# Kernel optimization log

Measured on AMD Instinct MI355X. Metric: run time of the kernel, lower is better.

The kernel has to match this reference:

```python
import jax, jax.numpy as jnp
import numpy as np

K = 2  # top-k experts per token

def setup_inputs() -> dict:
    key = jax.random.key(0)
    ks = jax.random.split(key, 8)
    B, S, D, F, E = 2, 1024, 1024, 4096, 8
    s_in = 1.0 / np.sqrt(D)
    s_mid = 1.0 / np.sqrt(F)
    return {
        "x": jax.random.normal(ks[0], (B, S, D), dtype=jnp.float32),
        "Wr": jax.random.uniform(ks[1], (D, E), jnp.float32, -s_in, s_in),
        "br": jax.random.uniform(ks[2], (E,), jnp.float32, -s_in, s_in),
        "W1": jax.random.uniform(ks[3], (E, D, F), jnp.float32, -s_in, s_in),
        "b1": jax.random.uniform(ks[4], (E, F), jnp.float32, -s_in, s_in),
        "W2": jax.random.uniform(ks[5], (E, F, D), jnp.float32, -s_mid, s_mid),
        "b2": jax.random.uniform(ks[6], (E, D), jnp.float32, -s_mid, s_mid),
    }

def _moe(x, Wr, br, W1, b1, W2, b2):
    E = Wr.shape[1]
    # router (eval mode: no noise)
    logits = jnp.einsum('bsd,de->bse', x, Wr) + br          # [B,S,E]
    topk_logits, topk_idx = jax.lax.top_k(logits, K)        # [B,S,K]
    router_probs = jax.nn.softmax(topk_logits, axis=-1)     # [B,S,K]
    # per-expert combine weight: sum over k slots assigned to expert e
    onehot = jax.nn.one_hot(topk_idx, E, dtype=x.dtype)     # [B,S,K,E]
    w = jnp.einsum('bske,bsk->bse', onehot, router_probs)   # [B,S,E]
    # scan over experts (fixed small E), accumulate weighted expert outputs
    def step(acc, ew):
        W1j, b1j, W2j, b2j, wj = ew                          # wj: [B,S]
        h = jax.nn.gelu(jnp.einsum('bsd,df->bsf', x, W1j) + b1j, approximate=False)
        y = jnp.einsum('bsf,fd->bsd', h, W2j) + b2j
        return acc + y * wj[..., None], None
    out, _ = jax.lax.scan(step, jnp.zeros_like(x),
                          (W1, b1, W2, b2, jnp.transpose(w, (2, 0, 1))))
    return out, router_probs

def reference(x, Wr, br, W1, b1, W2, b2):
    return _moe(x, Wr, br, W1, b1, W2, b2)
```

## Files before the change

### kernel.cpp

```cpp
#include <hip/hip_runtime.h>
#include <hip/hip_bf16.h>
#include <cstdint>

#define TOKENS 2048
#define Dm 1024
#define Fm 4096
#define Em 8

typedef short s16x8 __attribute__((ext_vector_type(8)));
typedef float f32x4 __attribute__((ext_vector_type(4)));

#define GLOAD16(g, l) __builtin_amdgcn_global_load_lds(                     \
    (const __attribute__((address_space(1))) void*)(g),                     \
    (__attribute__((address_space(3))) void*)(l), 16, 0, 0)

__device__ __forceinline__ ushort f2bf(float f) {
  union { float f; uint32_t u; } v; v.f = f;
  uint32_t r = v.u + 0x7fffu + ((v.u >> 16) & 1u);
  return (ushort)(r >> 16);
}

__global__ void transcvt(const float* __restrict__ in, ushort* __restrict__ out,
                         int R, int C) {
  __shared__ float tile[32][33];
  int e = blockIdx.z;
  const float* src = in + (size_t)e * R * C;
  ushort* dst = out + (size_t)e * R * C;
  int c0 = blockIdx.x * 32, r0 = blockIdx.y * 32;
  int lr = threadIdx.x >> 5, lc = threadIdx.x & 31;
#pragma unroll
  for (int p = 0; p < 4; ++p) {
    int r = r0 + p * 8 + lr;
    tile[p * 8 + lr][lc] = src[(size_t)r * C + c0 + lc];
  }
  __syncthreads();
#pragma unroll
  for (int p = 0; p < 4; ++p) {
    int c = c0 + p * 8 + lr;
    dst[(size_t)c * R + r0 + lc] = f2bf(tile[lc][p * 8 + lr]);
  }
}

__global__ void router(const float* __restrict__ x, const float* __restrict__ Wr,
                       const float* __restrict__ br, float* __restrict__ probs,
                       int* __restrict__ e_sel, float* __restrict__ w_sel,
                       ushort* __restrict__ xb) {
  int t = blockIdx.x;
  const float4* xr4 = (const float4*)(x + (size_t)t * Dm);
  float4 v = xr4[threadIdx.x];
  ushort4 o;
  o.x = f2bf(v.x); o.y = f2bf(v.y); o.z = f2bf(v.z); o.w = f2bf(v.w);
  ((ushort4*)(xb + (size_t)t * Dm))[threadIdx.x] = o;

  int d0 = threadIdx.x * 4;
  const float4* wr4 = (const float4*)(Wr + (size_t)d0 * Em);
  float wv[4][8];
#pragma unroll
  for (int r = 0; r < 4; ++r) {
    float4 a = wr4[r * 2], b = wr4[r * 2 + 1];
    wv[r][0] = a.x; wv[r][1] = a.y; wv[r][2] = a.z; wv[r][3] = a.w;
    wv[r][4] = b.x; wv[r][5] = b.y; wv[r][6] = b.z; wv[r][7] = b.w;
  }
  float xs[4] = {v.x, v.y, v.z, v.w};
  float acc[Em];
#pragma unroll
  for (int e = 0; e < Em; ++e)
    acc[e] = xs[0] * wv[0][e] + xs[1] * wv[1][e] + xs[2] * wv[2][e] + xs[3] * wv[3][e];

#pragma unroll
  for (int off = 32; off >= 1; off >>= 1)
#pragma unroll
    for (int e = 0; e < Em; ++e) acc[e] += __shfl_down(acc[e], off);
  __shared__ float red[4][Em];
  int lane = threadIdx.x & 63, wid = threadIdx.x >> 6;
  if (lane == 0)
#pragma unroll
    for (int e = 0; e < Em; ++e) red[wid][e] = acc[e];
  __syncthreads();
  if (threadIdx.x == 0) {
    float lg[Em];
#pragma unroll
    for (int e = 0; e < Em; ++e)
      lg[e] = red[0][e] + red[1][e] + red[2][e] + red[3][e] + br[e];
    int i0 = 0;
    for (int e = 1; e < Em; ++e) if (lg[e] > lg[i0]) i0 = e;
    int i1 = -1;
    for (int e = 0; e < Em; ++e) {
      if (e == i0) continue;
      if (i1 < 0 || lg[e] > lg[i1]) i1 = e;
    }
    float d = lg[i1] - lg[i0];
    float tt = expf(d);
    float inv = 1.f / (1.f + tt);
    float p0 = inv, p1 = tt * inv;
    probs[t * 2] = p0; probs[t * 2 + 1] = p1;
    e_sel[t * 2] = i0; e_sel[t * 2 + 1] = i1;
    w_sel[t * 2] = p0; w_sel[t * 2 + 1] = p1;
  }
}

__global__ void build_lists(const int* __restrict__ e_sel, const float* __restrict__ w_sel,
                            int* __restrict__ tok_of_row, float* __restrict__ w_of_row,
                            int* __restrict__ base, int* __restrict__ npad,
                            int* __restrict__ ncnt) {
  __shared__ int cnt[Em], run[Em], sbase[Em];
  __shared__ int wsum[4][Em];
  int tid = threadIdx.x, lane = tid & 63, wid = tid >> 6;
  if (tid < Em) { cnt[tid] = 0; run[tid] = 0; }
  __syncthreads();
  for (int t = tid; t < TOKENS; t += 256) {
    atomicAdd(&cnt[e_sel[2 * t]], 1);
    atomicAdd(&cnt[e_sel[2 * t + 1]], 1);
  }
  __syncthreads();
  if (tid == 0) {
    int b = 0;
    for (int e = 0; e < Em; ++e) {
      base[e] = b; sbase[e] = b;
      int n = cnt[e]; ncnt[e] = n;
      int p = (n + 127) & ~127;
      npad[e] = p; b += p;
    }
  }
  __syncthreads();
  for (int c = 0; c < TOKENS / 256; ++c) {
    int t = c * 256 + tid;
    int e0 = e_sel[2 * t], e1 = e_sel[2 * t + 1];
    unsigned long long mm[Em];
#pragma unroll
    for (int e = 0; e < Em; ++e) {
      unsigned long long m0 = __ballot(e0 == e);
      unsigned long long m1 = __ballot(e1 == e);
      mm[e] = m0 | m1;
      if (lane == 0) wsum[wid][e] = __popcll(mm[e]);
    }
    __syncthreads();
    unsigned long long below = (1ull << lane) - 1ull;
    {
      int e = e0;
      int p = __popcll(mm[e] & below);
      int pre = 0;
      for (int w = 0; w < wid; ++w) pre += wsum[w][e];
      int row = sbase[e] + run[e] + pre + p;
      tok_of_row[row] = t; w_of_row[row] = w_sel[2 * t];
    }
    {
      int e = e1;
      int p = __popcll(mm[e] & below);
      int pre = 0;
      for (int w = 0; w < wid; ++w) pre += wsum[w][e];
      int row = sbase[e] + run[e] + pre + p;
      tok_of_row[row] = t; w_of_row[row] = w_sel[2 * t + 1];
    }
    __syncthreads();
    if (tid < Em) {
      int s = 0;
      for (int w = 0; w < 4; ++w) s += wsum[w][tid];
      run[tid] += s;
    }
    __syncthreads();
  }
  for (int e = 0; e < Em; ++e) {
    int n = cnt[e];
    int p = (n + 127) & ~127;
    for (int i = n + tid; i < p; i += 256) {
      tok_of_row[sbase[e] + i] = -1;
      w_of_row[sbase[e] + i] = 0.f;
    }
  }
}

__global__ void out_init(const int* __restrict__ e_sel, const float* __restrict__ w_sel,
                         const float* __restrict__ b2, float* __restrict__ out) {
  int t = blockIdx.x;
  int e0 = e_sel[2 * t], e1 = e_sel[2 * t + 1];
  float w0 = w_sel[2 * t], w1 = w_sel[2 * t + 1];
  const float4* p0 = (const float4*)(b2 + (size_t)e0 * Dm);
  const float4* p1 = (const float4*)(b2 + (size_t)e1 * Dm);
  float4* o = (float4*)(out + (size_t)t * Dm);
  for (int i = threadIdx.x; i < Dm / 4; i += 256) {
    float4 a = p0[i], b = p1[i];
    float4 r;
    r.x = w0 * a.x + w1 * b.x; r.y = w0 * a.y + w1 * b.y;
    r.z = w0 * a.z + w1 * b.z; r.w = w0 * a.w + w1 * b.w;
    o[i] = r;
  }
}

__global__ __launch_bounds__(256) void gemm1(
    const ushort* __restrict__ xb, const ushort* __restrict__ bmat,
    const float* __restrict__ b1, ushort* __restrict__ H,
    const int* __restrict__ tok_of_row, const int* __restrict__ base,
    const int* __restrict__ npad) {
  int e = blockIdx.y >> 4, rt = blockIdx.y & 15;
  int np = npad[e];
  if (rt * 128 >= np) return;
  int row0 = base[e] + rt * 128;
  int n0 = blockIdx.x * 128;
  __shared__ ushort As[128 * 32];
  __shared__ ushort Bs[128 * 32];
  __shared__ int toks[128];
  int tid = threadIdx.x, lane = tid & 63, wid = tid >> 6;
  if (tid < 128) toks[tid] = tok_of_row[row0 + tid];
  __syncthreads();
  int arow = tid >> 2, asub = tid & 3;
  int t0 = toks[arow];      if (t0 < 0) t0 = 0;
  int t1 = toks[64 + arow]; if (t1 < 0) t1 = 0;
  const ushort* sA0 = xb + (size_t)t0 * Dm + asub * 8;
  const ushort* sA1 = xb + (size_t)t1 * Dm + asub * 8;
  const ushort* sB0 = bmat + ((size_t)e * Fm + n0 + arow) * Dm + asub * 8;
  const ushort* sB1 = sB0 + (size_t)64 * Dm;
  char* ldA0 = (char*)As + wid * 1024;
  char* ldA1 = (char*)As + 4096 + wid * 1024;
  char* ldB0 = (char*)Bs + wid * 1024;
  char* ldB1 = (char*)Bs + 4096 + wid * 1024;
  int wr = wid >> 1, wc = wid & 1;
  const ushort* aB = As + ((size_t)(wr * 64 + (lane & 15)) * 32) + (lane >> 4) * 8;
  const ushort* bB = Bs + ((size_t)(wc * 64 + (lane & 15)) * 32) + (lane >> 4) * 8;
  f32x4 acc[4][4] = {};
  for (int kt = 0; kt < Dm / 32; ++kt) {
    GLOAD16(sA0, ldA0);
    GLOAD16(sA1, ldA1);
    GLOAD16(sB0, ldB0);
    GLOAD16(sB1, ldB1);
    sA0 += 32; sA1 += 32; sB0 += 32; sB1 += 32;
    __syncthreads();
    s16x8 av[4], bv[4];
#pragma unroll
    for (int m = 0; m < 4; ++m) av[m] = *(const s16x8*)(aB + m * 512);
#pragma unroll
    for (int n = 0; n < 4; ++n) bv[n] = *(const s16x8*)(bB + n * 512);
#pragma unroll
    for (int m = 0; m < 4; ++m)
#pragma unroll
      for (int n = 0; n < 4; ++n)
        acc[m][n] = __builtin_amdgcn_mfma_f32_16x16x32_bf16(av[m], bv[n], acc[m][n], 0, 0, 0);
    __syncthreads();
  }
  int rb = wr * 64 + ((lane >> 4) << 2);
  int cb = n0 + wc * 64 + (lane & 15);
#pragma unroll
  for (int n = 0; n < 4; ++n) {
    int col = cb + n * 16;
    float bias = b1[e * Fm + col];
#pragma unroll
    for (int m = 0; m < 4; ++m) {
      int r = row0 + rb + m * 16;
#pragma unroll
      for (int j = 0; j < 4; ++j) {
        float v = acc[m][n][j] + bias;
        float g = 0.5f * v * (1.f + erff(v * 0.70710678118654752f));
        H[(size_t)(r + j) * Fm + col] = f2bf(g);
      }
    }
  }
}

__global__ __launch_bounds__(256) void gemm2(
    const ushort* __restrict__ H, const ushort* __restrict__ bmat,
    const int* __restrict__ tok_of_row, const float* __restrict__ w_of_row,
    const int* __restrict__ base, const int* __restrict__ npad,
    float* __restrict__ out) {
  int e = blockIdx.y >> 4, rt = blockIdx.y & 15;
  int np = npad[e];
  if (rt * 128 >= np) return;
  int row0 = base[e] + rt * 128;
  int n0 = blockIdx.x * 128;
  int k0 = blockIdx.z * (Fm / 2);
  __shared__ ushort As[128 * 32];
  __shared__ ushort Bs[128 * 32];
  __shared__ int toks[128];
  __shared__ float wts[128];
  int tid = threadIdx.x, lane = tid & 63, wid = tid >> 6;
  if (tid < 128) {
    toks[tid] = tok_of_row[row0 + tid];
    wts[tid] = w_of_row[row0 + tid];
  }
  __syncthreads();
  int arow = tid >> 2, asub = tid & 3;
  const ushort* sA0 = H + (size_t)(row0 + arow) * Fm + k0 + asub * 8;
  const ushort* sA1 = sA0 + (size_t)64 * Fm;
  const ushort* sB0 = bmat + ((size_t)e * Dm + n0 + arow) * Fm + k0 + asub * 8;
  const ushort* sB1 = sB0 + (size_t)64 * Fm;
  char* ldA0 = (char*)As + wid * 1024;
  char* ldA1 = (char*)As + 4096 + wid * 1024;
  char* ldB0 = (char*)Bs + wid * 1024;
  char* ldB1 = (char*)Bs + 4096 + wid * 1024;
  int wr = wid >> 1, wc = wid & 1;
  const ushort* aB = As + ((size_t)(wr * 64 + (lane & 15)) * 32) + (lane >> 4) * 8;
  const ushort* bB = Bs + ((size_t)(wc * 64 + (lane & 15)) * 32) + (lane >> 4) * 8;
  f32x4 acc[4][4] = {};
  for (int kt = 0; kt < Fm / 2 / 32; ++kt) {
    GLOAD16(sA0, ldA0);
    GLOAD16(sA1, ldA1);
    GLOAD16(sB0, ldB0);
    GLOAD16(sB1, ldB1);
    sA0 += 32; sA1 += 32; sB0 += 32; sB1 += 32;
    __syncthreads();
    s16x8 av[4], bv[4];
#pragma unroll
    for (int m = 0; m < 4; ++m) av[m] = *(const s16x8*)(aB + m * 512);
#pragma unroll
    for (int n = 0; n < 4; ++n) bv[n] = *(const s16x8*)(bB + n * 512);
#pragma unroll
    for (int m = 0; m < 4; ++m)
#pragma unroll
      for (int n = 0; n < 4; ++n)
        acc[m][n] = __builtin_amdgcn_mfma_f32_16x16x32_bf16(av[m], bv[n], acc[m][n], 0, 0, 0);
    __syncthreads();
  }
  int rb = wr * 64 + ((lane >> 4) << 2);
  int cb = n0 + wc * 64 + (lane & 15);
#pragma unroll
  for (int n = 0; n < 4; ++n) {
    int col = cb + n * 16;
#pragma unroll
    for (int m = 0; m < 4; ++m) {
      int rl = rb + m * 16;
#pragma unroll
      for (int j = 0; j < 4; ++j) {
        int tok = toks[rl + j];
        if (tok >= 0)
          atomicAdd(&out[(size_t)tok * Dm + col], wts[rl + j] * acc[m][n][j]);
      }
    }
  }
}

extern "C" void kernel_launch(void* const* d_in, const int* in_sizes, int n_in,
                              void* d_out, int out_size, void* d_ws, size_t ws_size,
                              hipStream_t stream) {
  const float* x  = (const float*)d_in[0];
  const float* Wr = (const float*)d_in[1];
  const float* br = (const float*)d_in[2];
  const float* W1 = (const float*)d_in[3];
  const float* b1 = (const float*)d_in[4];
  const float* W2 = (const float*)d_in[5];
  const float* b2 = (const float*)d_in[6];
  float* out = (float*)d_out;
  float* probs = out + (size_t)TOKENS * Dm;

  char* ws = (char*)d_ws;
  ushort* Wt   = (ushort*)ws;
  ushort* Hbuf = (ushort*)(ws + 67108864);
  ushort* xb   = (ushort*)(ws + 109051904);
  int*   tok_of_row = (int*)(ws + 113246208);
  float* w_of_row   = (float*)(ws + 113266688);
  int*   e_sel      = (int*)(ws + 113287168);
  float* w_sel      = (float*)(ws + 113303552);
  int*   meta       = (int*)(ws + 113319936);

  transcvt<<<dim3(Fm / 32, Dm / 32, Em), 256, 0, stream>>>(W1, Wt, Dm, Fm);
  router<<<TOKENS, 256, 0, stream>>>(x, Wr, br, probs, e_sel, w_sel, xb);
  build_lists<<<1, 256, 0, stream>>>(e_sel, w_sel, tok_of_row, w_of_row,
                                     meta, meta + 8, meta + 16);
  out_init<<<TOKENS, 256, 0, stream>>>(e_sel, w_sel, b2, out);
  gemm1<<<dim3(32, 128), 256, 0, stream>>>(xb, Wt, b1, Hbuf, tok_of_row,
                                           meta, meta + 8);
  transcvt<<<dim3(Dm / 32, Fm / 32, Em), 256, 0, stream>>>(W2, Wt, Fm, Dm);
  gemm2<<<dim3(8, 128, 2), 256, 0, stream>>>(Hbuf, Wt, tok_of_row, w_of_row,
                                             meta, meta + 8, out);
}
```

Baseline: 275.7 us.

## Fuse prep kernels, overlap W2 transpose with gemm1 idle blocks, widen K-tile with swizzle

Merges the W1 transpose with the router into one launch, and merges list building with the output bias init into another. When the workspace is large enough, the W2 transpose/convert is done by gemm1's idle (unused expert-tile) blocks instead of a separate kernel. Both GEMMs now load a 64-wide K slice per stage into a 128x64 XOR-swizzled LDS tile to cut bank conflicts and halve barrier count. gemm1 stages its GELU output through LDS so H is written with 16-byte coalesced stores. The trade-offs are more LDS per block, which may lower occupancy, and load imbalance from idle blocks doing the transpose work.

```diff
diff --git a/kernel.cpp b/kernel.cpp
--- a/kernel.cpp
+++ b/kernel.cpp
@@ -22,30 +22,43 @@
 
 __global__ void transcvt(const float* __restrict__ in, ushort* __restrict__ out,
                          int R, int C) {
-  __shared__ float tile[32][33];
+  __shared__ float tile[32 * 33];
   int e = blockIdx.z;
   const float* src = in + (size_t)e * R * C;
   ushort* dst = out + (size_t)e * R * C;
   int c0 = blockIdx.x * 32, r0 = blockIdx.y * 32;
   int lr = threadIdx.x >> 5, lc = threadIdx.x & 31;
 #pragma unroll
-  for (int p = 0; p < 4; ++p) {
-    int r = r0 + p * 8 + lr;
-    tile[p * 8 + lr][lc] = src[(size_t)r * C + c0 + lc];
-  }
-  __syncthreads();
-#pragma unroll
-  for (int p = 0; p < 4; ++p) {
-    int c = c0 + p * 8 + lr;
-    dst[(size_t)c * R + r0 + lc] = f2bf(tile[lc][p * 8 + lr]);
-  }
-}
-
-__global__ void router(const float* __restrict__ x, const float* __restrict__ Wr,
-                       const float* __restrict__ br, float* __restrict__ probs,
-                       int* __restrict__ e_sel, float* __restrict__ w_sel,
-                       ushort* __restrict__ xb) {
-  int t = blockIdx.x;
+  for (int p = 0; p < 4; ++p)
+    tile[(p * 8 + lr) * 33 + lc] = src[(size_t)(r0 + p * 8 + lr) * C + c0 + lc];
+  __syncthreads();
+#pragma unroll
+  for (int p = 0; p < 4; ++p)
+    dst[(size_t)(c0 + p * 8 + lr) * R + r0 + lc] = f2bf(tile[lc * 33 + p * 8 + lr]);
+}
+
+__global__ void prep(const float* __restrict__ W1, ushort* __restrict__ W1T,
+                     const float* __restrict__ x, const float* __restrict__ Wr,
+                     const float* __restrict__ br, float* __restrict__ probs,
+                     int* __restrict__ e_sel, float* __restrict__ w_sel,
+                     ushort* __restrict__ xb) {
+  __shared__ float shf[32 * 33];
+  int b = blockIdx.x;
+  if (b < 32768) {
+    int cx = b & 127, ry = (b >> 7) & 31, e = b >> 12;
+    const float* src = W1 + ((size_t)e * Dm + ry * 32) * Fm + cx * 32;
+    int lr = threadIdx.x >> 5, lc = threadIdx.x & 31;
+#pragma unroll
+    for (int p = 0; p < 4; ++p)
+      shf[(p * 8 + lr) * 33 + lc] = src[(size_t)(p * 8 + lr) * Fm + lc];
+    __syncthreads();
+#pragma unroll
+    for (int p = 0; p < 4; ++p)
+      W1T[((size_t)e * Fm + cx * 32 + p * 8 + lr) * Dm + ry * 32 + lc] =
+          f2bf(shf[lc * 33 + p * 8 + lr]);
+    return;
+  }
+  int t = b - 32768;
   const float4* xr4 = (const float4*)(x + (size_t)t * Dm);
   float4 v = xr4[threadIdx.x];
   ushort4 o;
@@ -57,31 +70,30 @@
   float wv[4][8];
 #pragma unroll
   for (int r = 0; r < 4; ++r) {
-    float4 a = wr4[r * 2], b = wr4[r * 2 + 1];
+    float4 a = wr4[r * 2], bq = wr4[r * 2 + 1];
     wv[r][0] = a.x; wv[r][1] = a.y; wv[r][2] = a.z; wv[r][3] = a.w;
-    wv[r][4] = b.x; wv[r][5] = b.y; wv[r][6] = b.z; wv[r][7] = b.w;
+    wv[r][4] = bq.x; wv[r][5] = bq.y; wv[r][6] = bq.z; wv[r][7] = bq.w;
   }
   float xs[4] = {v.x, v.y, v.z, v.w};
   float acc[Em];
 #pragma unroll
   for (int e = 0; e < Em; ++e)
     acc[e] = xs[0] * wv[0][e] + xs[1] * wv[1][e] + xs[2] * wv[2][e] + xs[3] * wv[3][e];
-
 #pragma unroll
   for (int off = 32; off >= 1; off >>= 1)
 #pragma unroll
     for (int e = 0; e < Em; ++e) acc[e] += __shfl_down(acc[e], off);
-  __shared__ float red[4][Em];
+  float* red = shf;
   int lane = threadIdx.x & 63, wid = threadIdx.x >> 6;
   if (lane == 0)
 #pragma unroll
-    for (int e = 0; e < Em; ++e) red[wid][e] = acc[e];
+    for (int e = 0; e < Em; ++e) red[wid * 8 + e] = acc[e];
   __syncthreads();
   if (threadIdx.x == 0) {
     float lg[Em];
 #pragma unroll
     for (int e = 0; e < Em; ++e)
-      lg[e] = red[0][e] + red[1][e] + red[2][e] + red[3][e] + br[e];
+      lg[e] = red[e] + red[8 + e] + red[16 + e] + red[24 + e] + br[e];
     int i0 = 0;
     for (int e = 1; e < Em; ++e) if (lg[e] > lg[i0]) i0 = e;
     int i1 = -1;
@@ -92,20 +104,34 @@
     float d = lg[i1] - lg[i0];
     float tt = expf(d);
     float inv = 1.f / (1.f + tt);
-    float p0 = inv, p1 = tt * inv;
-    probs[t * 2] = p0; probs[t * 2 + 1] = p1;
+    probs[t * 2] = inv; probs[t * 2 + 1] = tt * inv;
     e_sel[t * 2] = i0; e_sel[t * 2 + 1] = i1;
-    w_sel[t * 2] = p0; w_sel[t * 2 + 1] = p1;
-  }
-}
-
-__global__ void build_lists(const int* __restrict__ e_sel, const float* __restrict__ w_sel,
-                            int* __restrict__ tok_of_row, float* __restrict__ w_of_row,
-                            int* __restrict__ base, int* __restrict__ npad,
-                            int* __restrict__ ncnt) {
+    w_sel[t * 2] = inv; w_sel[t * 2 + 1] = tt * inv;
+  }
+}
+
+__global__ void build2(const int* __restrict__ e_sel, const float* __restrict__ w_sel,
+                       int* __restrict__ tok_of_row, float* __restrict__ w_of_row,
+                       int* __restrict__ base, int* __restrict__ npad,
+                       const float* __restrict__ b2, float* __restrict__ out) {
+  int tid = threadIdx.x;
+  if (blockIdx.x != 0) {
+    int t = blockIdx.x - 1;
+    int e0 = e_sel[2 * t], e1 = e_sel[2 * t + 1];
+    float w0 = w_sel[2 * t], w1 = w_sel[2 * t + 1];
+    const float4* p0 = (const float4*)(b2 + (size_t)e0 * Dm);
+    const float4* p1 = (const float4*)(b2 + (size_t)e1 * Dm);
+    float4* o = (float4*)(out + (size_t)t * Dm);
+    float4 a = p0[tid], b = p1[tid];
+    float4 r;
+    r.x = w0 * a.x + w1 * b.x; r.y = w0 * a.y + w1 * b.y;
+    r.z = w0 * a.z + w1 * b.z; r.w = w0 * a.w + w1 * b.w;
+    o[tid] = r;
+    return;
+  }
   __shared__ int cnt[Em], run[Em], sbase[Em];
   __shared__ int wsum[4][Em];
-  int tid = threadIdx.x, lane = tid & 63, wid = tid >> 6;
+  int lane = tid & 63, wid = tid >> 6;
   if (tid < Em) { cnt[tid] = 0; run[tid] = 0; }
   __syncthreads();
   for (int t = tid; t < TOKENS; t += 256) {
@@ -117,7 +143,7 @@
     int b = 0;
     for (int e = 0; e < Em; ++e) {
       base[e] = b; sbase[e] = b;
-      int n = cnt[e]; ncnt[e] = n;
+      int n = cnt[e];
       int p = (n + 127) & ~127;
       npad[e] = p; b += p;
     }
@@ -170,147 +196,196 @@
   }
 }
 
-__global__ void out_init(const int* __restrict__ e_sel, const float* __restrict__ w_sel,
-                         const float* __restrict__ b2, float* __restrict__ out) {
-  int t = blockIdx.x;
-  int e0 = e_sel[2 * t], e1 = e_sel[2 * t + 1];
-  float w0 = w_sel[2 * t], w1 = w_sel[2 * t + 1];
-  const float4* p0 = (const float4*)(b2 + (size_t)e0 * Dm);
-  const float4* p1 = (const float4*)(b2 + (size_t)e1 * Dm);
-  float4* o = (float4*)(out + (size_t)t * Dm);
-  for (int i = threadIdx.x; i < Dm / 4; i += 256) {
-    float4 a = p0[i], b = p1[i];
-    float4 r;
-    r.x = w0 * a.x + w1 * b.x; r.y = w0 * a.y + w1 * b.y;
-    r.z = w0 * a.z + w1 * b.z; r.w = w0 * a.w + w1 * b.w;
-    o[i] = r;
-  }
-}
-
 __global__ __launch_bounds__(256) void gemm1(
-    const ushort* __restrict__ xb, const ushort* __restrict__ bmat,
+    const ushort* __restrict__ xb, const ushort* __restrict__ W1T,
     const float* __restrict__ b1, ushort* __restrict__ H,
     const int* __restrict__ tok_of_row, const int* __restrict__ base,
-    const int* __restrict__ npad) {
+    const int* __restrict__ npad,
+    const float* __restrict__ W2, ushort* __restrict__ W2T, int do_w2) {
+  __shared__ ushort sbuf[17408];
+  __shared__ int toks[128];
+  int tid = threadIdx.x, lane = tid & 63, wid = tid >> 6;
   int e = blockIdx.y >> 4, rt = blockIdx.y & 15;
-  int np = npad[e];
-  if (rt * 128 >= np) return;
+  int nt = npad[e] >> 7;
+  if (rt >= nt) {
+    if (!do_w2) return;
+    int act = 0, pre = 0;
+#pragma unroll
+    for (int e2 = 0; e2 < Em; ++e2) {
+      int n2 = npad[e2] >> 7;
+      act += n2;
+      if (e2 < e) pre += 16 - n2;
+    }
+    int idle_id = (pre + rt - nt) * 32 + blockIdx.x;
+    int total_idle = (128 - act) * 32;
+    float* ft = (float*)sbuf;
+    int lr = tid >> 5, lc = tid & 31;
+    for (int t = idle_id; t < 32768; t += total_idle) {
+      int x2 = t & 31, y2 = (t >> 5) & 127, e2 = t >> 12;
+      const float* src = W2 + ((size_t)e2 * Fm + y2 * 32) * Dm + x2 * 32;
+#pragma unroll
+      for (int p = 0; p < 4; ++p)
+        ft[(p * 8 + lr) * 33 + lc] = src[(size_t)(p * 8 + lr) * Dm + lc];
+      __syncthreads();
+#pragma unroll
+      for (int p = 0; p < 4; ++p)
+        W2T[((size_t)e2 * Dm + x2 * 32 + p * 8 + lr) * Fm + y2 * 32 + lc] =
+            f2bf(ft[lc * 33 + p * 8 + lr]);
+      __syncthreads();
+    }
+    return;
+  }
   int row0 = base[e] + rt * 128;
   int n0 = blockIdx.x * 128;
-  __shared__ ushort As[128 * 32];
-  __shared__ ushort Bs[128 * 32];
-  __shared__ int toks[128];
-  int tid = threadIdx.x, lane = tid & 63, wid = tid >> 6;
   if (tid < 128) toks[tid] = tok_of_row[row0 + tid];
   __syncthreads();
-  int arow = tid >> 2, asub = tid & 3;
-  int t0 = toks[arow];      if (t0 < 0) t0 = 0;
-  int t1 = toks[64 + arow]; if (t1 < 0) t1 = 0;
-  const ushort* sA0 = xb + (size_t)t0 * Dm + asub * 8;
-  const ushort* sA1 = xb + (size_t)t1 * Dm + asub * 8;
-  const ushort* sB0 = bmat + ((size_t)e * Fm + n0 + arow) * Dm + asub * 8;
-  const ushort* sB1 = sB0 + (size_t)64 * Dm;
-  char* ldA0 = (char*)As + wid * 1024;
-  char* ldA1 = (char*)As + 4096 + wid * 1024;
-  char* ldB0 = (char*)Bs + wid * 1024;
-  char* ldB1 = (char*)Bs + 4096 + wid * 1024;
-  int wr = wid >> 1, wc = wid & 1;
-  const ushort* aB = As + ((size_t)(wr * 64 + (lane & 15)) * 32) + (lane >> 4) * 8;
-  const ushort* bB = Bs + ((size_t)(wc * 64 + (lane & 15)) * 32) + (lane >> 4) * 8;
+  ushort* As = sbuf;
+  ushort* Bs = sbuf + 8192;
+  int sub = tid & 7, rl0 = tid >> 3;
+  const ushort *pa0, *pa1, *pa2, *pa3, *pb0, *pb1, *pb2, *pb3;
+#define MKPTR1(c, pa, pb) {                                                 \
+    int row = (c) * 32 + rl0; int r7 = row & 7;                             \
+    int tk = toks[row]; if (tk < 0) tk = 0;                                 \
+    int so = (sub ^ r7) << 3;                                               \
+    pa = xb + (size_t)tk * Dm + so;                                         \
+    pb = W1T + ((size_t)e * Fm + n0 + row) * Dm + so; }
+  MKPTR1(0, pa0, pb0)
+  MKPTR1(1, pa1, pb1)
+  MKPTR1(2, pa2, pb2)
+  MKPTR1(3, pa3, pb3)
+  char* la = (char*)sbuf + wid * 1024;
+  char* lb = (char*)sbuf + 16384 + wid * 1024;
+  int wr2 = wid >> 1, wc2 = wid & 1;
+  int g = lane >> 4, l7 = lane & 7;
+  int aidx = (wr2 * 64 + (lane & 15)) * 64 + ((g ^ l7) << 3);
+  int bidx = (wc2 * 64 + (lane & 15)) * 64 + ((g ^ l7) << 3);
   f32x4 acc[4][4] = {};
-  for (int kt = 0; kt < Dm / 32; ++kt) {
-    GLOAD16(sA0, ldA0);
-    GLOAD16(sA1, ldA1);
-    GLOAD16(sB0, ldB0);
-    GLOAD16(sB1, ldB1);
-    sA0 += 32; sA1 += 32; sB0 += 32; sB1 += 32;
-    __syncthreads();
-    s16x8 av[4], bv[4];
-#pragma unroll
-    for (int m = 0; m < 4; ++m) av[m] = *(const s16x8*)(aB + m * 512);
-#pragma unroll
-    for (int n = 0; n < 4; ++n) bv[n] = *(const s16x8*)(bB + n * 512);
-#pragma unroll
-    for (int m = 0; m < 4; ++m)
+  for (int kt = 0; kt < Dm / 64; ++kt) {
+    GLOAD16(pa0, la);
+    GLOAD16(pa1, la + 4096);
+    GLOAD16(pa2, la + 8192);
+    GLOAD16(pa3, la + 12288);
+    GLOAD16(pb0, lb);
+    GLOAD16(pb1, lb + 4096);
+    GLOAD16(pb2, lb + 8192);
+    GLOAD16(pb3, lb + 12288);
+    pa0 += 64; pa1 += 64; pa2 += 64; pa3 += 64;
+    pb0 += 64; pb1 += 64; pb2 += 64; pb3 += 64;
+    __syncthreads();
+#pragma unroll
+    for (int kk = 0; kk < 2; ++kk) {
+      s16x8 av[4], bv[4];
+#pragma unroll
+      for (int m = 0; m < 4; ++m)
+        av[m] = *(const s16x8*)(As + ((aidx + m * 1024) ^ (kk << 5)));
 #pragma unroll
       for (int n = 0; n < 4; ++n)
-        acc[m][n] = __builtin_amdgcn_mfma_f32_16x16x32_bf16(av[m], bv[n], acc[m][n], 0, 0, 0);
-    __syncthreads();
-  }
-  int rb = wr * 64 + ((lane >> 4) << 2);
-  int cb = n0 + wc * 64 + (lane & 15);
+        bv[n] = *(const s16x8*)(Bs + ((bidx + n * 1024) ^ (kk << 5)));
+#pragma unroll
+      for (int m = 0; m < 4; ++m)
+#pragma unroll
+        for (int n = 0; n < 4; ++n)
+          acc[m][n] = __builtin_amdgcn_mfma_f32_16x16x32_bf16(av[m], bv[n], acc[m][n], 0, 0, 0);
+    }
+    __syncthreads();
+  }
+  int crow = wr2 * 64 + g * 4;
+  int ccol = wc2 * 64 + (lane & 15);
 #pragma unroll
   for (int n = 0; n < 4; ++n) {
-    int col = cb + n * 16;
+    int col = n0 + ccol + n * 16;
     float bias = b1[e * Fm + col];
 #pragma unroll
     for (int m = 0; m < 4; ++m) {
-      int r = row0 + rb + m * 16;
 #pragma unroll
       for (int j = 0; j < 4; ++j) {
         float v = acc[m][n][j] + bias;
-        float g = 0.5f * v * (1.f + erff(v * 0.70710678118654752f));
-        H[(size_t)(r + j) * Fm + col] = f2bf(g);
+        float gl = 0.5f * v * (1.f + erff(v * 0.70710678118654752f));
+        sbuf[(crow + m * 16 + j) * 136 + ccol + n * 16] = f2bf(gl);
       }
     }
   }
+  __syncthreads();
+#pragma unroll
+  for (int q = 0; q < 8; ++q) {
+    int id = q * 256 + tid;
+    int r = id >> 4, ch = id & 15;
+    s16x8 vv = *(const s16x8*)(sbuf + r * 136 + ch * 8);
+    *(s16x8*)(H + (size_t)(row0 + r) * Fm + n0 + ch * 8) = vv;
+  }
 }
 
 __global__ __launch_bounds__(256) void gemm2(
-    const ushort* __restrict__ H, const ushort* __restrict__ bmat,
+    const ushort* __restrict__ H, const ushort* __restrict__ W2T,
     const int* __restrict__ tok_of_row, const float* __restrict__ w_of_row,
     const int* __restrict__ base, const int* __restrict__ npad,
     float* __restrict__ out) {
+  __shared__ ushort sbuf[16384];
+  __shared__ int toks[128];
+  __shared__ float wts[128];
+  int tid = threadIdx.x, lane = tid & 63, wid = tid >> 6;
   int e = blockIdx.y >> 4, rt = blockIdx.y & 15;
-  int np = npad[e];
-  if (rt * 128 >= np) return;
+  int nt = npad[e] >> 7;
+  if (rt >= nt) return;
   int row0 = base[e] + rt * 128;
   int n0 = blockIdx.x * 128;
   int k0 = blockIdx.z * (Fm / 2);
-  __shared__ ushort As[128 * 32];
-  __shared__ ushort Bs[128 * 32];
-  __shared__ int toks[128];
-  __shared__ float wts[128];
-  int tid = threadIdx.x, lane = tid & 63, wid = tid >> 6;
   if (tid < 128) {
     toks[tid] = tok_of_row[row0 + tid];
     wts[tid] = w_of_row[row0 + tid];
   }
   __syncthreads();
-  int arow = tid >> 2, asub = tid & 3;
-  const ushort* sA0 = H + (size_t)(row0 + arow) * Fm + k0 + asub * 8;
-  const ushort* sA1 = sA0 + (size_t)64 * Fm;
-  const ushort* sB0 = bmat + ((size_t)e * Dm + n0 + arow) * Fm + k0 + asub * 8;
-  const ushort* sB1 = sB0 + (size_t)64 * Fm;
-  char* ldA0 = (char*)As + wid * 1024;
-  char* ldA1 = (char*)As + 4096 + wid * 1024;
-  char* ldB0 = (char*)Bs + wid * 1024;
-  char* ldB1 = (char*)Bs + 4096 + wid * 1024;
-  int wr = wid >> 1, wc = wid & 1;
-  const ushort* aB = As + ((size_t)(wr * 64 + (lane & 15)) * 32) + (lane >> 4) * 8;
-  const ushort* bB = Bs + ((size_t)(wc * 64 + (lane & 15)) * 32) + (lane >> 4) * 8;
+  ushort* As = sbuf;
+  ushort* Bs = sbuf + 8192;
+  int sub = tid & 7, rl0 = tid >> 3;
+  const ushort *pa0, *pa1, *pa2, *pa3, *pb0, *pb1, *pb2, *pb3;
+#define MKPTR2(c, pa, pb) {                                                 \
+    int row = (c) * 32 + rl0; int r7 = row & 7;                             \
+    int so = (sub ^ r7) << 3;                                               \
+    pa = H + (size_t)(row0 + row) * Fm + k0 + so;                           \
+    pb = W2T + ((size_t)e * Dm + n0 + row) * Fm + k0 + so; }
+  MKPTR2(0, pa0, pb0)
+  MKPTR2(1, pa1, pb1)
+  MKPTR2(2, pa2, pb2)
+  MKPTR2(3, pa3, pb3)
+  char* la = (char*)sbuf + wid * 1024;
+  char* lb = (char*)sbuf + 16384 + wid * 1024;
+  int wr2 = wid >> 1, wc2 = wid & 1;
+  int g = lane >> 4, l7 = lane & 7;
+  int aidx = (wr2 * 64 + (lane & 15)) * 64 + ((g ^ l7) << 3);
+  int bidx = (wc2 * 64 + (lane & 15)) * 64 + ((g ^ l7) << 3);
   f32x4 acc[4][4] = {};
-  for (int kt = 0; kt < Fm / 2 / 32; ++kt) {
-    GLOAD16(sA0, ldA0);
-    GLOAD16(sA1, ldA1);
-    GLOAD16(sB0, ldB0);
-    GLOAD16(sB1, ldB1);
-    sA0 += 32; sA1 += 32; sB0 += 32; sB1 += 32;
-    __syncthreads();
-    s16x8 av[4], bv[4];
-#pragma unroll
-    for (int m = 0; m < 4; ++m) av[m] = *(const s16x8*)(aB + m * 512);
-#pragma unroll
-    for (int n = 0; n < 4; ++n) bv[n] = *(const s16x8*)(bB + n * 512);
-#pragma unroll
-    for (int m = 0; m < 4; ++m)
+  for (int kt = 0; kt < Fm / 2 / 64; ++kt) {
+    GLOAD16(pa0, la);
+    GLOAD16(pa1, la + 4096);
+    GLOAD16(pa2, la + 8192);
+    GLOAD16(pa3, la + 12288);
+    GLOAD16(pb0, lb);
+    GLOAD16(pb1, lb + 4096);
+    GLOAD16(pb2, lb + 8192);
+    GLOAD16(pb3, lb + 12288);
+    pa0 += 64; pa1 += 64; pa2 += 64; pa3 += 64;
+    pb0 += 64; pb1 += 64; pb2 += 64; pb3 += 64;
+    __syncthreads();
+#pragma unroll
+    for (int kk = 0; kk < 2; ++kk) {
+      s16x8 av[4], bv[4];
+#pragma unroll
+      for (int m = 0; m < 4; ++m)
+        av[m] = *(const s16x8*)(As + ((aidx + m * 1024) ^ (kk << 5)));
 #pragma unroll
       for (int n = 0; n < 4; ++n)
-        acc[m][n] = __builtin_amdgcn_mfma_f32_16x16x32_bf16(av[m], bv[n], acc[m][n], 0, 0, 0);
-    __syncthreads();
-  }
-  int rb = wr * 64 + ((lane >> 4) << 2);
-  int cb = n0 + wc * 64 + (lane & 15);
+        bv[n] = *(const s16x8*)(Bs + ((bidx + n * 1024) ^ (kk << 5)));
+#pragma unroll
+      for (int m = 0; m < 4; ++m)
+#pragma unroll
+        for (int n = 0; n < 4; ++n)
+          acc[m][n] = __builtin_amdgcn_mfma_f32_16x16x32_bf16(av[m], bv[n], acc[m][n], 0, 0, 0);
+    }
+    __syncthreads();
+  }
+  int rb = wr2 * 64 + g * 4;
+  int cb = n0 + wc2 * 64 + (lane & 15);
 #pragma unroll
   for (int n = 0; n < 4; ++n) {
     int col = cb + n * 16;
@@ -341,7 +416,7 @@
   float* probs = out + (size_t)TOKENS * Dm;
 
   char* ws = (char*)d_ws;
-  ushort* Wt   = (ushort*)ws;
+  ushort* W1T  = (ushort*)ws;
   ushort* Hbuf = (ushort*)(ws + 67108864);
   ushort* xb   = (ushort*)(ws + 109051904);
   int*   tok_of_row = (int*)(ws + 113246208);
@@ -349,15 +424,16 @@
   int*   e_sel      = (int*)(ws + 113287168);
   float* w_sel      = (float*)(ws + 113303552);
   int*   meta       = (int*)(ws + 113319936);
-
-  transcvt<<<dim3(Fm / 32, Dm / 32, Em), 256, 0, stream>>>(W1, Wt, Dm, Fm);
-  router<<<TOKENS, 256, 0, stream>>>(x, Wr, br, probs, e_sel, w_sel, xb);
-  build_lists<<<1, 256, 0, stream>>>(e_sel, w_sel, tok_of_row, w_of_row,
-                                     meta, meta + 8, meta + 16);
-  out_init<<<TOKENS, 256, 0, stream>>>(e_sel, w_sel, b2, out);
-  gemm1<<<dim3(32, 128), 256, 0, stream>>>(xb, Wt, b1, Hbuf, tok_of_row,
-                                           meta, meta + 8);
-  transcvt<<<dim3(Dm / 32, Fm / 32, Em), 256, 0, stream>>>(W2, Wt, Fm, Dm);
-  gemm2<<<dim3(8, 128, 2), 256, 0, stream>>>(Hbuf, Wt, tok_of_row, w_of_row,
+  int sep = (ws_size >= 180429056ULL) ? 1 : 0;
+  ushort* W2T = sep ? (ushort*)(ws + 113320192) : W1T;
+
+  prep<<<32768 + TOKENS, 256, 0, stream>>>(W1, W1T, x, Wr, br, probs, e_sel, w_sel, xb);
+  build2<<<TOKENS + 1, 256, 0, stream>>>(e_sel, w_sel, tok_of_row, w_of_row,
+                                         meta, meta + 8, b2, out);
+  gemm1<<<dim3(32, 128), 256, 0, stream>>>(xb, W1T, b1, Hbuf, tok_of_row,
+                                           meta, meta + 8, W2, W2T, sep);
+  if (!sep)
+    transcvt<<<dim3(Dm / 32, Fm / 32, Em), 256, 0, stream>>>(W2, W2T, Fm, Dm);
+  gemm2<<<dim3(8, 128, 2), 256, 0, stream>>>(Hbuf, W2T, tok_of_row, w_of_row,
                                              meta, meta + 8, out);
 }
```

Measured after the change: 313.7 us. +13.8%, slower.
